# Optimization experiments

Measured on AMD Instinct MI355X. Metric: run time of the kernel, lower is better.

## Reference

```python
import jax, jax.numpy as jnp
import numpy as np

B, T, E, A = 4, 4096, 512, 64

def setup_inputs() -> dict:
    key = jax.random.key(0)
    k1, k2, k3, k4 = jax.random.split(key, 4)
    embedded = jax.random.normal(k1, (B, T, E), dtype=jnp.float32)
    # torch Linear(E, A, bias=False): weight [A, E], y = x @ W.T. Store as [E, A].
    s = 1.0 / np.sqrt(E)
    Wq = jax.random.uniform(k2, (E, A), dtype=jnp.float32, minval=-s, maxval=s)
    Wk = jax.random.uniform(k3, (E, A), dtype=jnp.float32, minval=-s, maxval=s)
    Wv = jax.random.uniform(k4, (E, A), dtype=jnp.float32, minval=-s, maxval=s)
    return {"embedded": embedded, "Wq": Wq, "Wk": Wk, "Wv": Wv}

def reference(embedded, Wq, Wk, Wv):
    Q = embedded @ Wq  # [B, T, A]
    K = embedded @ Wk
    V = embedded @ Wv
    A_dim = V.shape[-1]
    scores = jnp.einsum('btd,bsd->bts', Q, K) / jnp.sqrt(jnp.float32(A_dim))  # [B, T, T]
    Tlen = scores.shape[-1]
    causal = jnp.tril(jnp.ones((Tlen, Tlen), dtype=bool))
    scores = jnp.where(causal, scores, -jnp.inf)
    attn = jax.nn.softmax(scores, axis=-1)
    out = jnp.einsum('bts,bsd->btd', attn, V)  # [B, T, A]
    return jnp.round(out, 4)
```

## Files before the change

### kernel.cpp

```cpp
#include <hip/hip_runtime.h>

#define B_ 4
#define T_ 4096
#define E_ 512
#define A_ 64
#define SQSCALE 0.1803368801111204f

typedef __attribute__((ext_vector_type(8)))  short bf16x8;
typedef __attribute__((ext_vector_type(8)))  unsigned short ushort8;
typedef __attribute__((ext_vector_type(4)))  unsigned int   u32x4;
typedef __attribute__((ext_vector_type(4)))  float f32x4;
typedef __attribute__((ext_vector_type(16))) float f32x16;

__device__ __forceinline__ unsigned short f2bf(float x) {
    union { float f; unsigned int u; } v; v.f = x;
    unsigned int r = v.u + 0x7fffu + ((v.u >> 16) & 1u);
    return (unsigned short)(r >> 16);
}
__device__ __forceinline__ unsigned cvtpk(float a, float b) {
    unsigned r;
    asm("v_cvt_pk_bf16_f32 %0, %1, %2" : "=v"(r) : "v"(a), "v"(b));
    return r;
}
__device__ __forceinline__ void pls(unsigned &a, unsigned &b) {
    asm("v_permlane32_swap_b32 %0, %1" : "+v"(a), "+v"(b));
}

__global__ __launch_bounds__(256) void prep_w(
    const float* __restrict__ Wq, const float* __restrict__ Wk,
    const float* __restrict__ Wv, unsigned short* __restrict__ Wp)
{
    const int e = blockIdx.x * 256 + threadIdx.x;
    const int nt = e >> 10;
    const int ks = (e >> 6) & 15;
    const int l  = e & 63;
    const int col = nt * 16 + (l & 15);
    const int kb  = ks * 32 + (l >> 4) * 8;
    const float* W = (col < 64) ? Wq : ((col < 128) ? Wk : Wv);
    const int cc = col & 63;
    const float sc = (col < 64) ? SQSCALE : 1.f;
    union { unsigned short s[8]; ushort8 v; } u;
    #pragma unroll
    for (int j = 0; j < 8; ++j) u.s[j] = f2bf(W[(kb + j) * 64 + cc] * sc);
    *(ushort8*)&Wp[(size_t)e * 8] = u.v;
}

__global__ __launch_bounds__(512, 4) void qkv_proj_kernel(
    const float* __restrict__ emb, const unsigned short* __restrict__ Wp,
    unsigned short* __restrict__ Qp, unsigned short* __restrict__ Kp,
    unsigned short* __restrict__ Vp)
{
    __shared__ unsigned short at[32][536];
    __shared__ unsigned short qt[32][72];
    __shared__ unsigned short kt[32][72];
    __shared__ unsigned short vt[64][40];
    const int tid = threadIdx.x;
    const long row0 = (long)blockIdx.x * 32;

    {
        const int r = tid >> 4, c16 = tid & 15;
        const float* __restrict__ src = emb + (row0 + r) * 512;
        #pragma unroll
        for (int j = 0; j < 4; ++j) {
            const int col = j * 128 + c16 * 8;
            const float4 x0 = *(const float4*)(src + col);
            const float4 x1 = *(const float4*)(src + col + 4);
            u32x4 p;
            p[0] = cvtpk(x0.x, x0.y); p[1] = cvtpk(x0.z, x0.w);
            p[2] = cvtpk(x1.x, x1.y); p[3] = cvtpk(x1.z, x1.w);
            *(u32x4*)&at[r][col] = p;
        }
    }
    __syncthreads();

    const int w = tid >> 6, lane = tid & 63;
    const int c = lane & 15, hi = lane >> 4;
    const int rg = w & 1, ng = w >> 1;

    f32x4 acc[3];
    #pragma unroll
    for (int j = 0; j < 3; ++j) acc[j] = (f32x4){0.f, 0.f, 0.f, 0.f};

    #pragma unroll
    for (int ks = 0; ks < 16; ++ks) {
        const bf16x8 af = *(const bf16x8*)&at[rg * 16 + c][ks * 32 + hi * 8];
        #pragma unroll
        for (int j = 0; j < 3; ++j) {
            const int nt = ng * 3 + j;
            const bf16x8 bf_ = *(const bf16x8*)&Wp[((size_t)(nt * 16 + ks) * 64 + lane) * 8];
            acc[j] = __builtin_amdgcn_mfma_f32_16x16x32_bf16(af, bf_, acc[j], 0, 0, 0);
        }
    }

    #pragma unroll
    for (int j = 0; j < 3; ++j) {
        const int nt = ng * 3 + j;
        #pragma unroll
        for (int r4 = 0; r4 < 4; ++r4) {
            const int rloc = rg * 16 + hi * 4 + r4;
            const unsigned short v = f2bf(acc[j][r4]);
            if (nt < 4)       qt[rloc][nt * 16 + c] = v;
            else if (nt < 8)  kt[rloc][(nt - 4) * 16 + c] = v;
            else              vt[(nt - 8) * 16 + c][rloc] = v;
        }
    }
    __syncthreads();

    const int tloc = (int)(row0 & 4095);
    const long bb = row0 >> 12;
    const int ci  = tloc >> 6;
    const int f_  = (tloc >> 5) & 1;
    const int ks0 = (tloc >> 4) & 3;
    const int tt  = tloc >> 5;
    if (tid < 256) {
        const int kk = tid >> 6, l = tid & 63;
        const ushort8 kval = *(const ushort8*)&kt[l & 31][kk * 16 + (l >> 5) * 8];
        *(ushort8*)&Kp[((((bb * 64 + ci) * 2 + f_) * 4 + kk) * 64 + l) * 8] = kval;
        const ushort8 qval = *(const ushort8*)&qt[l & 31][kk * 16 + (l >> 5) * 8];
        *(ushort8*)&Qp[(((bb * 128 + tt) * 4 + kk) * 64 + l) * 8] = qval;
    } else {
        const int e = tid - 256;
        const int ksl = e >> 7, ct = (e >> 6) & 1, l = e & 63;
        const ushort8 val = *(const ushort8*)&vt[ct * 32 + (l & 31)][ksl * 16 + (l >> 5) * 8];
        *(ushort8*)&Vp[((((bb * 64 + ci) * 4 + ks0 + ksl) * 2 + ct) * 64 + l) * 8] = val;
    }
}

__global__ __launch_bounds__(512, 1) void attn_kernel(
    const unsigned short* __restrict__ Qp, const unsigned short* __restrict__ Kp,
    const unsigned short* __restrict__ Vp, float* __restrict__ out)
{
    __shared__ float accbuf[8][32][68];
    __shared__ float mbuf[8][32], lbuf[8][32];

    const int tid = threadIdx.x, w = tid >> 6, lane = tid & 63;
    const int c = lane & 31, h = lane >> 5;
    const int b = blockIdx.x & 3;
    const int pp = blockIdx.x >> 2;

    const unsigned short* __restrict__ Qpb = Qp + (size_t)b * 128 * 4 * 512;
    const unsigned short* __restrict__ Kpb = Kp + (size_t)b * 64 * 8 * 512;
    const unsigned short* __restrict__ Vpb = Vp + (size_t)b * 64 * 8 * 512;

    for (int ti = 0; ti < 2; ++ti) {
        const int t = ti ? pp : (127 - pp);
        const int qb = t << 5;
        const int nc = ((qb + 31) >> 6) + 1;

        bf16x8 qf[4];
        #pragma unroll
        for (int kk = 0; kk < 4; ++kk)
            qf[kk] = *(const bf16x8*)&Qpb[(((size_t)t * 4 + kk) * 64 + lane) * 8];

        f32x16 acc[2];
        #pragma unroll
        for (int ct = 0; ct < 2; ++ct)
            #pragma unroll
            for (int j = 0; j < 16; ++j) acc[ct][j] = 0.f;
        float m = -1e30f, l = 0.f;

        const unsigned short* kptr = Kpb + (size_t)w * 4096 + lane * 8;
        const unsigned short* vptr = Vpb + (size_t)w * 4096 + lane * 8;

        bf16x8 kf[2][4];
        {
            const unsigned short* kp0 = (w < nc) ? kptr : (kptr - (size_t)(w - nc + 1) * 4096);
            #pragma unroll
            for (int f = 0; f < 2; ++f)
                #pragma unroll
                for (int kk = 0; kk < 4; ++kk)
                    kf[f][kk] = *(const bf16x8*)&kp0[f * 2048 + kk * 512];
        }

        for (int ci = w; ci < nc; ci += 8) {
            const int s0 = ci << 6;

            bf16x8 vf[4][2];
            #pragma unroll
            for (int ks = 0; ks < 4; ++ks)
                #pragma unroll
                for (int ct = 0; ct < 2; ++ct)
                    vf[ks][ct] = *(const bf16x8*)&vptr[ks * 1024 + ct * 512];

            f32x16 sf[2];
            #pragma unroll
            for (int f = 0; f < 2; ++f)
                #pragma unroll
                for (int j = 0; j < 16; ++j) sf[f][j] = 0.f;
            __builtin_amdgcn_s_setprio(1);
            #pragma unroll
            for (int f = 0; f < 2; ++f)
                #pragma unroll
                for (int kk = 0; kk < 4; ++kk)
                    sf[f] = __builtin_amdgcn_mfma_f32_32x32x16_bf16(kf[f][kk], qf[kk], sf[f], 0, 0, 0);
            __builtin_amdgcn_s_setprio(0);

            const unsigned short* knp = (ci + 8 < nc) ? (kptr + 32768) : kptr;
            bf16x8 kn[2][4];
            #pragma unroll
            for (int f = 0; f < 2; ++f)
                #pragma unroll
                for (int kk = 0; kk < 4; ++kk)
                    kn[f][kk] = *(const bf16x8*)&knp[f * 2048 + kk * 512];

            if (s0 + 63 > qb) {
                #pragma unroll
                for (int f = 0; f < 2; ++f)
                    #pragma unroll
                    for (int r = 0; r < 16; ++r) {
                        const int key = s0 + f * 32 + ((r & 3) + 8 * (r >> 2)) + 4 * h;
                        if (key > qb + c) sf[f][r] = -1e30f;
                    }
            }

            float t0 = fmaxf(sf[0][0], sf[1][0]);
            float t1 = fmaxf(sf[0][1], sf[1][1]);
            float t2 = fmaxf(sf[0][2], sf[1][2]);
            float t3 = fmaxf(sf[0][3], sf[1][3]);
            #pragma unroll
            for (int r = 4; r < 16; r += 4) {
                t0 = fmaxf(t0, fmaxf(sf[0][r],     sf[1][r]));
                t1 = fmaxf(t1, fmaxf(sf[0][r + 1], sf[1][r + 1]));
                t2 = fmaxf(t2, fmaxf(sf[0][r + 2], sf[1][r + 2]));
                t3 = fmaxf(t3, fmaxf(sf[0][r + 3], sf[1][r + 3]));
            }
            float pm = fmaxf(fmaxf(t0, t1), fmaxf(t2, t3));
            pm = fmaxf(pm, __shfl_xor(pm, 32));

            float mn = m;
            if (__any(pm > m)) {
                mn = fmaxf(m, pm);
                const float sc = exp2f(m - mn);
                m = mn;
                l *= sc;
                #pragma unroll
                for (int ct = 0; ct < 2; ++ct)
                    #pragma unroll
                    for (int r = 0; r < 16; ++r) acc[ct][r] *= sc;
            }

            float s0a = 0.f, s1a = 0.f, s2a = 0.f, s3a = 0.f;
            #pragma unroll
            for (int f = 0; f < 2; ++f)
                #pragma unroll
                for (int r = 0; r < 16; r += 4) {
                    float p0 = exp2f(sf[f][r] - mn);
                    float p1 = exp2f(sf[f][r + 1] - mn);
                    float p2 = exp2f(sf[f][r + 2] - mn);
                    float p3 = exp2f(sf[f][r + 3] - mn);
                    sf[f][r] = p0; sf[f][r + 1] = p1; sf[f][r + 2] = p2; sf[f][r + 3] = p3;
                    s0a += p0; s1a += p1; s2a += p2; s3a += p3;
                }
            float rs = (s0a + s1a) + (s2a + s3a);
            rs += __shfl_xor(rs, 32);
            l += rs;

            #pragma unroll
            for (int f = 0; f < 2; ++f) {
                unsigned w01 = cvtpk(sf[f][0], sf[f][1]);
                unsigned w23 = cvtpk(sf[f][2], sf[f][3]);
                unsigned w45 = cvtpk(sf[f][4], sf[f][5]);
                unsigned w67 = cvtpk(sf[f][6], sf[f][7]);
                pls(w01, w45); pls(w23, w67);
                union { unsigned uu[4]; bf16x8 v; } pa0, pa1;
                pa0.uu[0] = w01; pa0.uu[1] = w23; pa0.uu[2] = w45; pa0.uu[3] = w67;
                unsigned x01 = cvtpk(sf[f][8],  sf[f][9]);
                unsigned x23 = cvtpk(sf[f][10], sf[f][11]);
                unsigned x45 = cvtpk(sf[f][12], sf[f][13]);
                unsigned x67 = cvtpk(sf[f][14], sf[f][15]);
                pls(x01, x45); pls(x23, x67);
                pa1.uu[0] = x01; pa1.uu[1] = x23; pa1.uu[2] = x45; pa1.uu[3] = x67;
                __builtin_amdgcn_s_setprio(1);
                #pragma unroll
                for (int ct = 0; ct < 2; ++ct) {
                    acc[ct] = __builtin_amdgcn_mfma_f32_32x32x16_bf16(vf[2 * f][ct],     pa0.v, acc[ct], 0, 0, 0);
                    acc[ct] = __builtin_amdgcn_mfma_f32_32x32x16_bf16(vf[2 * f + 1][ct], pa1.v, acc[ct], 0, 0, 0);
                }
                __builtin_amdgcn_s_setprio(0);
            }

            #pragma unroll
            for (int f = 0; f < 2; ++f)
                #pragma unroll
                for (int kk = 0; kk < 4; ++kk) kf[f][kk] = kn[f][kk];
            kptr += 32768;
            vptr += 32768;
        }

        if (h == 0) { mbuf[w][c] = m; lbuf[w][c] = l; }
        #pragma unroll
        for (int ct = 0; ct < 2; ++ct)
            #pragma unroll
            for (int g = 0; g < 4; ++g)
                *(float4*)&accbuf[w][c][ct * 32 + g * 8 + 4 * h] =
                    make_float4(acc[ct][4 * g], acc[ct][4 * g + 1],
                                acc[ct][4 * g + 2], acc[ct][4 * g + 3]);
        __syncthreads();
        #pragma unroll
        for (int i = 0; i < 4; ++i) {
            const int e = tid + i * 512;
            const int q = e >> 6, d = e & 63;
            float ms = mbuf[0][q];
            #pragma unroll
            for (int wv = 1; wv < 8; ++wv) ms = fmaxf(ms, mbuf[wv][q]);
            float ls = 0.f, os = 0.f;
            #pragma unroll
            for (int wv = 0; wv < 8; ++wv) {
                const float e_ = exp2f(mbuf[wv][q] - ms);
                ls += lbuf[wv][q] * e_;
                os += accbuf[wv][q][d] * e_;
            }
            out[((long)b * T_ + qb + q) * 64 + d] = os / ls;
        }
        __syncthreads();
    }
}

extern "C" void kernel_launch(void* const* d_in, const int* in_sizes, int n_in,
                              void* d_out, int out_size, void* d_ws, size_t ws_size,
                              hipStream_t stream)
{
    const float* emb = (const float*)d_in[0];
    const float* Wq  = (const float*)d_in[1];
    const float* Wk  = (const float*)d_in[2];
    const float* Wv  = (const float*)d_in[3];
    float* out = (float*)d_out;

    unsigned short* Qp = (unsigned short*)d_ws;
    unsigned short* Kp = Qp + (size_t)B_ * T_ * A_;
    unsigned short* Vp = Kp + (size_t)B_ * T_ * A_;
    unsigned short* Wp = Vp + (size_t)B_ * T_ * A_;

    prep_w<<<dim3(48), dim3(256), 0, stream>>>(Wq, Wk, Wv, Wp);
    qkv_proj_kernel<<<dim3(512), dim3(512), 0, stream>>>(emb, Wp, Qp, Kp, Vp);
    attn_kernel<<<dim3(256), dim3(512), 0, stream>>>(Qp, Kp, Vp, out);
}
```

Baseline: 46.22 us.

## Double QKV projection row tile to 64 and alias LDS buffers

The QKV projection now gives each block 64 rows instead of 32, which halves the grid to 256 blocks. Each wave computes two 16-row tiles, so every weight fragment read from global memory feeds two MFMAs. The Q/K/V staging buffers now reuse the input tile's LDS region, which needs an extra barrier after the MFMA loop. Launch bounds drop to 1 block per SM, and the larger LDS footprint and fewer blocks may reduce occupancy and latency hiding.

```diff
diff --git a/kernel.cpp b/kernel.cpp
--- a/kernel.cpp
+++ b/kernel.cpp
@@ -45,24 +45,25 @@
     *(ushort8*)&Wp[(size_t)e * 8] = u.v;
 }
 
-__global__ __launch_bounds__(512, 4) void qkv_proj_kernel(
+__global__ __launch_bounds__(512, 1) void qkv_proj_kernel(
     const float* __restrict__ emb, const unsigned short* __restrict__ Wp,
     unsigned short* __restrict__ Qp, unsigned short* __restrict__ Kp,
     unsigned short* __restrict__ Vp)
 {
-    __shared__ unsigned short at[32][536];
-    __shared__ unsigned short qt[32][72];
-    __shared__ unsigned short kt[32][72];
-    __shared__ unsigned short vt[64][40];
+    __shared__ unsigned short lds[64 * 536];
+    unsigned short (*at)[536] = (unsigned short (*)[536])lds;
+    unsigned short (*qt)[72]  = (unsigned short (*)[72])lds;
+    unsigned short (*kt)[72]  = (unsigned short (*)[72])(lds + 4608);
+    unsigned short (*vt)[72]  = (unsigned short (*)[72])(lds + 9216);
     const int tid = threadIdx.x;
-    const long row0 = (long)blockIdx.x * 32;
+    const long row0 = (long)blockIdx.x * 64;
 
     {
-        const int r = tid >> 4, c16 = tid & 15;
+        const int r = tid >> 3, c8 = tid & 7;
         const float* __restrict__ src = emb + (row0 + r) * 512;
         #pragma unroll
-        for (int j = 0; j < 4; ++j) {
-            const int col = j * 128 + c16 * 8;
+        for (int j = 0; j < 8; ++j) {
+            const int col = j * 64 + c8 * 8;
             const float4 x0 = *(const float4*)(src + col);
             const float4 x1 = *(const float4*)(src + col + 4);
             u32x4 p;
@@ -75,54 +76,59 @@
 
     const int w = tid >> 6, lane = tid & 63;
     const int c = lane & 15, hi = lane >> 4;
-    const int rg = w & 1, ng = w >> 1;
-
-    f32x4 acc[3];
+    const int rg2 = w >> 2, ng = w & 3;
+
+    f32x4 acc[2][3];
     #pragma unroll
-    for (int j = 0; j < 3; ++j) acc[j] = (f32x4){0.f, 0.f, 0.f, 0.f};
+    for (int rr = 0; rr < 2; ++rr)
+        #pragma unroll
+        for (int j = 0; j < 3; ++j) acc[rr][j] = (f32x4){0.f, 0.f, 0.f, 0.f};
 
     #pragma unroll
     for (int ks = 0; ks < 16; ++ks) {
-        const bf16x8 af = *(const bf16x8*)&at[rg * 16 + c][ks * 32 + hi * 8];
+        const bf16x8 a0 = *(const bf16x8*)&at[rg2 * 32 + c][ks * 32 + hi * 8];
+        const bf16x8 a1 = *(const bf16x8*)&at[rg2 * 32 + 16 + c][ks * 32 + hi * 8];
         #pragma unroll
         for (int j = 0; j < 3; ++j) {
             const int nt = ng * 3 + j;
             const bf16x8 bf_ = *(const bf16x8*)&Wp[((size_t)(nt * 16 + ks) * 64 + lane) * 8];
-            acc[j] = __builtin_amdgcn_mfma_f32_16x16x32_bf16(af, bf_, acc[j], 0, 0, 0);
-        }
-    }
+            acc[0][j] = __builtin_amdgcn_mfma_f32_16x16x32_bf16(a0, bf_, acc[0][j], 0, 0, 0);
+            acc[1][j] = __builtin_amdgcn_mfma_f32_16x16x32_bf16(a1, bf_, acc[1][j], 0, 0, 0);
+        }
+    }
+    __syncthreads();
 
     #pragma unroll
     for (int j = 0; j < 3; ++j) {
         const int nt = ng * 3 + j;
         #pragma unroll
-        for (int r4 = 0; r4 < 4; ++r4) {
-            const int rloc = rg * 16 + hi * 4 + r4;
-            const unsigned short v = f2bf(acc[j][r4]);
-            if (nt < 4)       qt[rloc][nt * 16 + c] = v;
-            else if (nt < 8)  kt[rloc][(nt - 4) * 16 + c] = v;
-            else              vt[(nt - 8) * 16 + c][rloc] = v;
-        }
+        for (int rr = 0; rr < 2; ++rr)
+            #pragma unroll
+            for (int r4 = 0; r4 < 4; ++r4) {
+                const int rloc = rg2 * 32 + rr * 16 + hi * 4 + r4;
+                const unsigned short v = f2bf(acc[rr][j][r4]);
+                if (nt < 4)       qt[rloc][nt * 16 + c] = v;
+                else if (nt < 8)  kt[rloc][(nt - 4) * 16 + c] = v;
+                else              vt[(nt - 8) * 16 + c][rloc] = v;
+            }
     }
     __syncthreads();
 
-    const int tloc = (int)(row0 & 4095);
     const long bb = row0 >> 12;
-    const int ci  = tloc >> 6;
-    const int f_  = (tloc >> 5) & 1;
-    const int ks0 = (tloc >> 4) & 3;
-    const int tt  = tloc >> 5;
-    if (tid < 256) {
-        const int kk = tid >> 6, l = tid & 63;
-        const ushort8 kval = *(const ushort8*)&kt[l & 31][kk * 16 + (l >> 5) * 8];
-        *(ushort8*)&Kp[((((bb * 64 + ci) * 2 + f_) * 4 + kk) * 64 + l) * 8] = kval;
-        const ushort8 qval = *(const ushort8*)&qt[l & 31][kk * 16 + (l >> 5) * 8];
-        *(ushort8*)&Qp[(((bb * 128 + tt) * 4 + kk) * 64 + l) * 8] = qval;
-    } else {
-        const int e = tid - 256;
-        const int ksl = e >> 7, ct = (e >> 6) & 1, l = e & 63;
-        const ushort8 val = *(const ushort8*)&vt[ct * 32 + (l & 31)][ksl * 16 + (l >> 5) * 8];
-        *(ushort8*)&Vp[((((bb * 64 + ci) * 4 + ks0 + ksl) * 2 + ct) * 64 + l) * 8] = val;
+    const int ci  = (int)(row0 & 4095) >> 6;
+    const int tt0 = (int)(row0 & 4095) >> 5;
+    const int l = tid & 63;
+    {
+        const int f = tid >> 8, kk = (tid >> 6) & 3;
+        const ushort8 kval = *(const ushort8*)&kt[f * 32 + (l & 31)][kk * 16 + (l >> 5) * 8];
+        *(ushort8*)&Kp[((((bb * 64 + ci) * 2 + f) * 4 + kk) * 64 + l) * 8] = kval;
+        const ushort8 qval = *(const ushort8*)&qt[f * 32 + (l & 31)][kk * 16 + (l >> 5) * 8];
+        *(ushort8*)&Qp[(((bb * 128 + tt0 + f) * 4 + kk) * 64 + l) * 8] = qval;
+    }
+    {
+        const int ks_ = tid >> 7, ct = (tid >> 6) & 1;
+        const ushort8 vval = *(const ushort8*)&vt[ct * 32 + (l & 31)][ks_ * 16 + (l >> 5) * 8];
+        *(ushort8*)&Vp[((((bb * 64 + ci) * 4 + ks_) * 2 + ct) * 64 + l) * 8] = vval;
     }
 }
 
@@ -332,6 +338,6 @@
     unsigned short* Wp = Vp + (size_t)B_ * T_ * A_;
 
     prep_w<<<dim3(48), dim3(256), 0, stream>>>(Wq, Wk, Wv, Wp);
-    qkv_proj_kernel<<<dim3(512), dim3(512), 0, stream>>>(emb, Wp, Qp, Kp, Vp);
+    qkv_proj_kernel<<<dim3(256), dim3(512), 0, stream>>>(emb, Wp, Qp, Kp, Vp);
     attn_kernel<<<dim3(256), dim3(512), 0, stream>>>(Qp, Kp, Vp, out);
 }
```

Measured after the change: 47.63 us. 1.03x slower.
